# Kernel optimization log

Hardware: AMD Instinct MI355X
Metric: run time of the kernel (lower is better)

The kernel has to match this reference:

```python
import jax, jax.numpy as jnp
import numpy as np

EMBED_DIM = 1024
B, S = 8, 4096

def setup_inputs() -> dict:
    key = jax.random.key(0)
    k_x, k_w1, k_b1, k_phi, k_w2, k_b2 = jax.random.split(key, 6)
    lim1 = 1.0 / np.sqrt(EMBED_DIM)
    lim2 = 1.0  # linear2 fan_in = ffn_dim = 1
    return {
        "x": jax.random.normal(k_x, (B, S, EMBED_DIM), dtype=jnp.float32),
        "W1": jax.random.uniform(k_w1, (1, EMBED_DIM), jnp.float32, -lim1, lim1),
        "b1": jax.random.uniform(k_b1, (1,), jnp.float32, -lim1, lim1),
        "phi": jax.random.uniform(k_phi, (), jnp.float32, 0.0, 2.0 * np.pi),
        "W2": jax.random.uniform(k_w2, (EMBED_DIM, 1), jnp.float32, -lim2, lim2),
        "b2": jax.random.uniform(k_b2, (EMBED_DIM,), jnp.float32, -lim2, lim2),
    }

def reference(x, W1, b1, phi, W2, b2):
    # linear1: per-token projection to a scalar angle theta  [B,S,1]
    theta = jnp.einsum("bsd,od->bso", x, W1) + b1
    # 1-qubit circuit RY(theta) -> RX(phi) -> <PauliZ> on |0>
    # closed form: <Z> = cos(theta) * cos(phi)
    q = jnp.cos(theta) * jnp.cos(phi)  # [B,S,1]
    # dropout=0 (eval); linear2: ffn_dim(=1) -> embed_dim
    out = jnp.einsum("bso,do->bsd", q, W2) + b2  # [B,S,EMBED_DIM]
    return out
```

## Files before the change

kernel.cpp:

```cpp
#include <hip/hip_runtime.h>
#include <math.h>


#define EMBED_D 1024
#define NTOK    (8 * 4096)
#define TPW     4
#define TOK_PER_BLOCK (4 * TPW)

typedef float f4 __attribute__((ext_vector_type(4)));

__global__ __launch_bounds__(256) void ffq_kernel(
    const float* __restrict__ x,
    const float* __restrict__ W1,
    const float* __restrict__ b1,
    const float* __restrict__ phi,
    const float* __restrict__ W2,
    const float* __restrict__ b2,
    float* __restrict__ out)
{
    const int lane = threadIdx.x & 63;
    const int wib  = threadIdx.x >> 6;
    const int tok0 = (blockIdx.x * 4 + wib) * TPW;

    const f4* xb = (const f4*)x + (size_t)tok0 * (EMBED_D / 4);
    f4 xv[TPW][4];
    #pragma unroll
    for (int t = 0; t < TPW; ++t)
        #pragma unroll
        for (int c = 0; c < 4; ++c)
            xv[t][c] = xb[t * (EMBED_D / 4) + c * 64 + lane];

    const f4* w14 = (const f4*)W1;
    const f4* w24 = (const f4*)W2;
    const f4* b24 = (const f4*)b2;
    f4 w1r[4], w2r[4], b2r[4];
    #pragma unroll
    for (int c = 0; c < 4; ++c) {
        w1r[c] = w14[c * 64 + lane];
        w2r[c] = w24[c * 64 + lane];
        b2r[c] = b24[c * 64 + lane];
    }
    const float cphi = cosf(phi[0]);
    const float b1v  = b1[0];

    float v[TPW];
    #pragma unroll
    for (int t = 0; t < TPW; ++t) {
        float s = 0.f;
        #pragma unroll
        for (int c = 0; c < 4; ++c) {
            s = fmaf(xv[t][c].x, w1r[c].x, s);
            s = fmaf(xv[t][c].y, w1r[c].y, s);
            s = fmaf(xv[t][c].z, w1r[c].z, s);
            s = fmaf(xv[t][c].w, w1r[c].w, s);
        }
        v[t] = s;
    }

    #pragma unroll
    for (int m = 32; m > 0; m >>= 1) {
        #pragma unroll
        for (int t = 0; t < TPW; ++t)
            v[t] += __shfl_xor(v[t], m, 64);
    }

    float q[TPW];
    #pragma unroll
    for (int t = 0; t < TPW; ++t)
        q[t] = cosf(v[t] + b1v) * cphi;

    f4* ob = (f4*)out + (size_t)tok0 * (EMBED_D / 4);
    #pragma unroll
    for (int t = 0; t < TPW; ++t) {
        #pragma unroll
        for (int c = 0; c < 4; ++c) {
            f4 o;
            o.x = fmaf(q[t], w2r[c].x, b2r[c].x);
            o.y = fmaf(q[t], w2r[c].y, b2r[c].y);
            o.z = fmaf(q[t], w2r[c].z, b2r[c].z);
            o.w = fmaf(q[t], w2r[c].w, b2r[c].w);
            __builtin_nontemporal_store(o, &ob[t * (EMBED_D / 4) + c * 64 + lane]);
        }
    }
}

extern "C" void kernel_launch(void* const* d_in, const int* in_sizes, int n_in,
                              void* d_out, int out_size, void* d_ws, size_t ws_size,
                              hipStream_t stream) {
    const float* x   = (const float*)d_in[0];
    const float* W1  = (const float*)d_in[1];
    const float* b1  = (const float*)d_in[2];
    const float* phi = (const float*)d_in[3];
    const float* W2  = (const float*)d_in[4];
    const float* b2  = (const float*)d_in[5];
    float* out = (float*)d_out;

    ffq_kernel<<<NTOK / TOK_PER_BLOCK, 256, 0, stream>>>(x, W1, b1, phi, W2, b2, out);
}
```

Before: 245.9 us.

## Stream x rows through LDS with a depth-4 async load pipeline per wave

Each wave now handles 16 rows instead of 4 and keeps four rows in flight. It stages them into LDS with global_load_lds, and hand-tuned vmcnt waits overlap the next row's loads with the current row's dot product and output stores. The aim is to hide HBM latency and cut register pressure while keeping the kernel bandwidth-bound. The change also drops nontemporal stores and launches four times fewer blocks. The hardcoded vmcnt counts are fragile, since stores also increment vmcnt, and the smaller grid may leave fewer waves to hide latency.

```diff
diff --git a/kernel.cpp b/kernel.cpp
--- a/kernel.cpp
+++ b/kernel.cpp
@@ -4,12 +4,68 @@
 
 #define EMBED_D 1024
 #define NTOK    (8 * 4096)
-#define TPW     4
-#define TOK_PER_BLOCK (4 * TPW)
+#define ROWS    16
+#define DEPTH   4
 
 typedef float f4 __attribute__((ext_vector_type(4)));
 
-__global__ __launch_bounds__(256) void ffq_kernel(
+#define WAITVM(n) asm volatile("s_waitcnt vmcnt(" #n ")" ::: "memory")
+
+__device__ __forceinline__ void stage16(const float* g, float* l) {
+    __builtin_amdgcn_global_load_lds(
+        (const __attribute__((address_space(1))) float*)g,
+        (__attribute__((address_space(3))) float*)l,
+        16, 0, 0);
+}
+
+__device__ __forceinline__ void stage_row(const float* xrow, float* lslot, int lane) {
+    #pragma unroll
+    for (int s = 0; s < 4; ++s)
+        stage16(xrow + s * 256 + lane * 4, lslot + s * 256);
+}
+
+__device__ __forceinline__ float row_dot(const f4* lr, int lane, const f4* w1r) {
+    float s = 0.f;
+    #pragma unroll
+    for (int c = 0; c < 4; ++c) {
+        f4 xv = lr[c * 64 + lane];
+        s = fmaf(xv.x, w1r[c].x, s);
+        s = fmaf(xv.y, w1r[c].y, s);
+        s = fmaf(xv.z, w1r[c].z, s);
+        s = fmaf(xv.w, w1r[c].w, s);
+    }
+    return s;
+}
+
+#define ROW_STEP(i, W)                                                      \
+  do {                                                                      \
+    WAITVM(W);                                                              \
+    __builtin_amdgcn_sched_barrier(0);                                      \
+    float sd = row_dot((const f4*)(lw + ((i) & (DEPTH - 1)) * EMBED_D),     \
+                       lane, w1r);                                          \
+    sd += __shfl_xor(sd, 32, 64);                                           \
+    sd += __shfl_xor(sd, 16, 64);                                           \
+    sd += __shfl_xor(sd, 8, 64);                                            \
+    sd += __shfl_xor(sd, 4, 64);                                            \
+    sd += __shfl_xor(sd, 2, 64);                                            \
+    sd += __shfl_xor(sd, 1, 64);                                            \
+    const float q = cosf(sd + b1v) * cphi;                                  \
+    f4* orow = (f4*)(out + (size_t)(row0 + (i)) * EMBED_D);                 \
+    _Pragma("unroll")                                                       \
+    for (int c = 0; c < 4; ++c) {                                           \
+      f4 o;                                                                 \
+      o.x = fmaf(q, w2r[c].x, b2r[c].x);                                    \
+      o.y = fmaf(q, w2r[c].y, b2r[c].y);                                    \
+      o.z = fmaf(q, w2r[c].z, b2r[c].z);                                    \
+      o.w = fmaf(q, w2r[c].w, b2r[c].w);                                    \
+      orow[c * 64 + lane] = o;                                              \
+    }                                                                       \
+    if ((i) + DEPTH < ROWS)                                                 \
+      stage_row(x + (size_t)(row0 + (i) + DEPTH) * EMBED_D,                 \
+                lw + ((i) & (DEPTH - 1)) * EMBED_D, lane);                  \
+  } while (0)
+
+__global__ __launch_bounds__(256) void ffq_fused(
     const float* __restrict__ x,
     const float* __restrict__ W1,
     const float* __restrict__ b1,
@@ -20,15 +76,10 @@
 {
     const int lane = threadIdx.x & 63;
     const int wib  = threadIdx.x >> 6;
-    const int tok0 = (blockIdx.x * 4 + wib) * TPW;
+    const int row0 = (blockIdx.x * 4 + wib) * ROWS;
 
-    const f4* xb = (const f4*)x + (size_t)tok0 * (EMBED_D / 4);
-    f4 xv[TPW][4];
-    #pragma unroll
-    for (int t = 0; t < TPW; ++t)
-        #pragma unroll
-        for (int c = 0; c < 4; ++c)
-            xv[t][c] = xb[t * (EMBED_D / 4) + c * 64 + lane];
+    __shared__ __attribute__((aligned(16))) float lds[4 * DEPTH * EMBED_D];
+    float* lw = lds + wib * DEPTH * EMBED_D;
 
     const f4* w14 = (const f4*)W1;
     const f4* w24 = (const f4*)W2;
@@ -40,48 +91,33 @@
         w2r[c] = w24[c * 64 + lane];
         b2r[c] = b24[c * 64 + lane];
     }
+    const float b1v  = b1[0];
     const float cphi = cosf(phi[0]);
-    const float b1v  = b1[0];
 
-    float v[TPW];
-    #pragma unroll
-    for (int t = 0; t < TPW; ++t) {
-        float s = 0.f;
-        #pragma unroll
-        for (int c = 0; c < 4; ++c) {
-            s = fmaf(xv[t][c].x, w1r[c].x, s);
-            s = fmaf(xv[t][c].y, w1r[c].y, s);
-            s = fmaf(xv[t][c].z, w1r[c].z, s);
-            s = fmaf(xv[t][c].w, w1r[c].w, s);
-        }
-        v[t] = s;
-    }
+    __builtin_amdgcn_sched_barrier(0);
 
     #pragma unroll
-    for (int m = 32; m > 0; m >>= 1) {
-        #pragma unroll
-        for (int t = 0; t < TPW; ++t)
-            v[t] += __shfl_xor(v[t], m, 64);
-    }
+    for (int d = 0; d < DEPTH; ++d)
+        stage_row(x + (size_t)(row0 + d) * EMBED_D, lw + d * EMBED_D, lane);
 
-    float q[TPW];
-    #pragma unroll
-    for (int t = 0; t < TPW; ++t)
-        q[t] = cosf(v[t] + b1v) * cphi;
+    __builtin_amdgcn_sched_barrier(0);
 
-    f4* ob = (f4*)out + (size_t)tok0 * (EMBED_D / 4);
-    #pragma unroll
-    for (int t = 0; t < TPW; ++t) {
-        #pragma unroll
-        for (int c = 0; c < 4; ++c) {
-            f4 o;
-            o.x = fmaf(q[t], w2r[c].x, b2r[c].x);
-            o.y = fmaf(q[t], w2r[c].y, b2r[c].y);
-            o.z = fmaf(q[t], w2r[c].z, b2r[c].z);
-            o.w = fmaf(q[t], w2r[c].w, b2r[c].w);
-            __builtin_nontemporal_store(o, &ob[t * (EMBED_D / 4) + c * 64 + lane]);
-        }
-    }
+    ROW_STEP(0, 12);
+    ROW_STEP(1, 16);
+    ROW_STEP(2, 20);
+    ROW_STEP(3, 24);
+    ROW_STEP(4, 24);
+    ROW_STEP(5, 24);
+    ROW_STEP(6, 24);
+    ROW_STEP(7, 24);
+    ROW_STEP(8, 24);
+    ROW_STEP(9, 24);
+    ROW_STEP(10, 24);
+    ROW_STEP(11, 24);
+    ROW_STEP(12, 24);
+    ROW_STEP(13, 20);
+    ROW_STEP(14, 16);
+    ROW_STEP(15, 12);
 }
 
 extern "C" void kernel_launch(void* const* d_in, const int* in_sizes, int n_in,
@@ -95,5 +131,5 @@
     const float* b2  = (const float*)d_in[5];
     float* out = (float*)d_out;
 
-    ffq_kernel<<<NTOK / TOK_PER_BLOCK, 256, 0, stream>>>(x, W1, b1, phi, W2, b2, out);
+    ffq_fused<<<NTOK / (4 * ROWS), 256, 0, stream>>>(x, W1, b1, phi, W2, b2, out);
 }
```

After: 248.2 us. About the same (+0.9%).
